# Performance work log

Measured on AMD Instinct MI355X. Metric: run time of the kernel, lower is better.

The kernel has to match this reference:

```python
import jax, jax.numpy as jnp
import numpy as np

IN_FEATURES = 4096
OUT_FEATURES = 4096
GROUP_SIZE = 128
TOKENS = 8192


def setup_inputs() -> dict:
    key = jax.random.key(0)
    k1, k2, k3 = jax.random.split(key, 3)
    x = jax.random.normal(k1, (TOKENS, IN_FEATURES), dtype=jnp.float32)
    weight_packed = jax.random.randint(k2, (OUT_FEATURES, IN_FEATURES // 2), 0, 256, dtype=jnp.int32)
    num_groups = IN_FEATURES // GROUP_SIZE
    weight_scales = jax.random.uniform(k3, (OUT_FEATURES, num_groups), dtype=jnp.float32) * 0.02
    return {"x": x, "weight_packed": weight_packed, "weight_scales": weight_scales, "group_size": GROUP_SIZE}


def _dequantize_int4(packed, scales, group_size):
    # packed: [N, K//2] int (uint8 values); scales: [N, G]
    out_features = packed.shape[0]
    in_features = packed.shape[1] * 2
    low = (packed & 15) - 8   # even columns
    high = ((packed >> 4) & 15) - 8  # odd columns
    # interleave low/high along last axis -> [N, K]
    unpacked = jnp.stack([low, high], axis=-1).reshape(out_features, in_features)
    num_groups = in_features // group_size
    w = unpacked.reshape(out_features, num_groups, group_size).astype(scales.dtype)
    w = w * scales[:, :, None]  # per-group scale
    return w.reshape(out_features, in_features)


def reference(x, weight_packed, weight_scales, group_size):
    W = _dequantize_int4(weight_packed, weight_scales, group_size)  # [N, K]
    # nn.functional.linear: x @ W.T (bias=False)
    return jnp.einsum('tk,nk->tn', x, W)
```

## Files before the change

kernel.cpp:

```cpp
#include <hip/hip_runtime.h>
#include <cstdint>
#include <cstddef>

#define TOKENS 8192
#define IN_F   4096
#define OUT_F  4096

typedef __bf16 bf16;
typedef bf16  bf16x8 __attribute__((ext_vector_type(8)));
typedef float f32x4  __attribute__((ext_vector_type(4)));

__global__ void prep_kernel(const float* __restrict__ xin, bf16* __restrict__ xout,
                            const int* __restrict__ wp, const float* __restrict__ sc,
                            bf16* __restrict__ wout) {
    if (blockIdx.x < 16384) {
        size_t i = ((size_t)blockIdx.x * 256 + threadIdx.x) * 8;
        const float4* p = (const float4*)(xin + i);
        float4 a = p[0], b = p[1];
        bf16x8 r;
        r[0] = (bf16)a.x; r[1] = (bf16)a.y; r[2] = (bf16)a.z; r[3] = (bf16)a.w;
        r[4] = (bf16)b.x; r[5] = (bf16)b.y; r[6] = (bf16)b.z; r[7] = (bf16)b.w;
        *(bf16x8*)(xout + i) = r;
    } else {
        int t  = (blockIdx.x - 16384) * 256 + threadIdx.x;
        int j0 = t << 2;
        int n  = j0 >> 11;
        int g  = (j0 & 2047) >> 6;
        float s = sc[(n << 5) + g];
        int4 p = *(const int4*)(wp + j0);
        bf16x8 r;
        r[0] = (bf16)((float)((p.x & 15) - 8) * s);
        r[1] = (bf16)((float)(((p.x >> 4) & 15) - 8) * s);
        r[2] = (bf16)((float)((p.y & 15) - 8) * s);
        r[3] = (bf16)((float)(((p.y >> 4) & 15) - 8) * s);
        r[4] = (bf16)((float)((p.z & 15) - 8) * s);
        r[5] = (bf16)((float)(((p.z >> 4) & 15) - 8) * s);
        r[6] = (bf16)((float)((p.w & 15) - 8) * s);
        r[7] = (bf16)((float)(((p.w >> 4) & 15) - 8) * s);
        *(bf16x8*)(wout + ((size_t)j0 << 1)) = r;
    }
}


#define GLL(src, dst) __builtin_amdgcn_global_load_lds( \
    (const __attribute__((address_space(1))) void*)(src), \
    (__attribute__((address_space(3))) void*)(dst), 16, 0, 0)
#define BAR() asm volatile("s_barrier" ::: "memory")

__global__ __launch_bounds__(512, 2)
void gemm_kernel(const bf16* __restrict__ A, const bf16* __restrict__ B,
                 float* __restrict__ C) {
    __shared__ char smem[131072] __attribute__((aligned(128)));

    const int tid  = threadIdx.x;
    const int lane = tid & 63;
    const int w    = tid >> 6;
    const int wr   = w >> 2, wc = w & 3;
    const int lrow = lane >> 3;
    const int gsw  = (lane & 7) ^ lrow;

    const int wg = ((blockIdx.x & 7) << 6) | (blockIdx.x >> 3);
    const int mt = wg >> 4;
    const int nt = wg & 15;

    const char* Abase = (const char*)A + (size_t)(mt * 256) * (IN_F * 2);
    const char* Bbase = (const char*)B + (size_t)(nt * 256) * (IN_F * 2);

    const char* gA[4];
#pragma unroll
    for (int t = 0; t < 4; ++t)
        gA[t] = Abase + (size_t)(t * 64 + w * 8 + lrow) * (IN_F * 2) + gsw * 16;
    const int rb = (w >> 2) * 64 + (w & 3) * 8;
    const int brow0 = rb, brow1 = rb + 128, brow2 = rb + 32, brow3 = rb + 160;
    const char* gB[4];
    gB[0] = Bbase + (size_t)(brow0 + lrow) * (IN_F * 2) + gsw * 16;
    gB[1] = Bbase + (size_t)(brow1 + lrow) * (IN_F * 2) + gsw * 16;
    gB[2] = Bbase + (size_t)(brow2 + lrow) * (IN_F * 2) + gsw * 16;
    gB[3] = Bbase + (size_t)(brow3 + lrow) * (IN_F * 2) + gsw * 16;

    char* const sm = smem;
#define ST_A0(b, kt) { GLL(gA[0] + (kt) * 128, sm + (b) * 65536 +     0 + w * 1024); \
                       GLL(gA[2] + (kt) * 128, sm + (b) * 65536 + 16384 + w * 1024); }
#define ST_A1(b, kt) { GLL(gA[1] + (kt) * 128, sm + (b) * 65536 +  8192 + w * 1024); \
                       GLL(gA[3] + (kt) * 128, sm + (b) * 65536 + 24576 + w * 1024); }
#define ST_B0(b, kt) { GLL(gB[0] + (kt) * 128, sm + (b) * 65536 + 32768 + brow0 * 128); \
                       GLL(gB[1] + (kt) * 128, sm + (b) * 65536 + 32768 + brow1 * 128); }
#define ST_B1(b, kt) { GLL(gB[2] + (kt) * 128, sm + (b) * 65536 + 32768 + brow2 * 128); \
                       GLL(gB[3] + (kt) * 128, sm + (b) * 65536 + 32768 + brow3 * 128); }

    const int m_lane = lane & 15, quad = lane >> 4, sw = m_lane & 7;
    const bf16x8* pA0 = (const bf16x8*)sm;
    const bf16x8* pB0 = (const bf16x8*)(sm + 32768);
    const bf16x8* pA1 = (const bf16x8*)(sm + 65536);
    const bf16x8* pB1 = (const bf16x8*)(sm + 98304);

    f32x4 acc[8][4];
#pragma unroll
    for (int i = 0; i < 8; ++i)
#pragma unroll
        for (int j = 0; j < 4; ++j) acc[i][j] = (f32x4)0.0f;

    ST_A0(0, 0); ST_B0(0, 0); ST_B1(0, 0); ST_A1(0, 0);
    ST_A0(1, 1); ST_B0(1, 1); ST_B1(1, 1);
    asm volatile("s_waitcnt vmcnt(6)" ::: "memory");
    BAR();

#define LDA(PA, qr) \
    { _Pragma("unroll") for (int i = 0; i < 4; ++i) { \
        _Pragma("unroll") for (int kh = 0; kh < 2; ++kh) { \
            af[i][kh] = (PA)[(wr * 128 + ((qr) * 4 + i) * 16 + m_lane) * 8 + ((kh * 4 + quad) ^ sw)]; } } }
#define LDB(PB) \
    { _Pragma("unroll") for (int j = 0; j < 4; ++j) { \
        _Pragma("unroll") for (int kh = 0; kh < 2; ++kh) { \
            bfr[j][kh] = (PB)[(wc * 64 + j * 16 + m_lane) * 8 + ((kh * 4 + quad) ^ sw)]; } } }
#define MM(qr, qc) \
    { __builtin_amdgcn_s_setprio(1); \
      _Pragma("unroll") for (int i = 0; i < 4; ++i) { \
        _Pragma("unroll") for (int j = 0; j < 2; ++j) { \
          _Pragma("unroll") for (int kh = 0; kh < 2; ++kh) { \
            acc[(qr) * 4 + i][(qc) * 2 + j] = __builtin_amdgcn_mfma_f32_16x16x32_bf16( \
                af[i][kh], bfr[(qc) * 2 + j][kh], acc[(qr) * 4 + i][(qc) * 2 + j], 0, 0, 0); } } } \
      __builtin_amdgcn_s_setprio(0); }

    for (int it = 0; it < 32; ++it) {
        const int kt0 = 2 * it;
        const int kt1 = kt0 + 1;
        const bool more = (it < 31);
        {
            bf16x8 af[4][2], bfr[4][2];
            LDA(pA0, 0); LDB(pB0);
            ST_A1(1, kt1);
            BAR(); MM(0, 0); BAR();
            if (more) ST_A0(0, kt0 + 2);
            BAR(); MM(0, 1); BAR();
            LDA(pA0, 1);
            if (more) ST_B0(0, kt0 + 2);
            BAR(); MM(1, 0); BAR();
            if (more) ST_B1(0, kt0 + 2);
            if (more) { asm volatile("s_waitcnt vmcnt(6)" ::: "memory"); }
            else      { asm volatile("s_waitcnt vmcnt(0)" ::: "memory"); }
            BAR(); MM(1, 1); BAR();
        }
        {
            bf16x8 af[4][2], bfr[4][2];
            LDA(pA1, 0); LDB(pB1);
            if (more) ST_A1(0, kt1 + 1);
            BAR(); MM(0, 0); BAR();
            if (more) ST_A0(1, kt1 + 2);
            BAR(); MM(0, 1); BAR();
            LDA(pA1, 1);
            if (more) ST_B0(1, kt1 + 2);
            BAR(); MM(1, 0); BAR();
            if (more) ST_B1(1, kt1 + 2);
            if (more) { asm volatile("s_waitcnt vmcnt(6)" ::: "memory"); }
            BAR(); MM(1, 1); BAR();
        }
    }

    const size_t crow0 = (size_t)(mt * 256 + wr * 128 + quad * 4) * OUT_F
                       + (size_t)(nt * 256 + wc * 64 + m_lane);
#pragma unroll
    for (int i = 0; i < 8; ++i)
#pragma unroll
        for (int r = 0; r < 4; ++r) {
            float* cp = C + crow0 + (size_t)(i * 16 + r) * OUT_F;
#pragma unroll
            for (int j = 0; j < 4; ++j) cp[j * 16] = acc[i][j][r];
        }
}

__global__ void naive_kernel(const float* __restrict__ x, const int* __restrict__ wp,
                             const float* __restrict__ sc, float* __restrict__ out) {
    int o = blockIdx.x * 256 + threadIdx.x;
    int t = o >> 12, n = o & 4095;
    const float* xr = x + (size_t)t * IN_F;
    const int*   wr2 = wp + (size_t)n * (IN_F / 2);
    float acc = 0.f;
    for (int g = 0; g < 32; ++g) {
        float s = sc[n * 32 + g];
        float part = 0.f;
        for (int j = 0; j < 64; ++j) {
            int p = wr2[g * 64 + j];
            part += xr[g * 128 + 2 * j]     * (float)((p & 15) - 8);
            part += xr[g * 128 + 2 * j + 1] * (float)(((p >> 4) & 15) - 8);
        }
        acc += part * s;
    }
    out[o] = acc;
}

extern "C" void kernel_launch(void* const* d_in, const int* in_sizes, int n_in,
                              void* d_out, int out_size, void* d_ws, size_t ws_size,
                              hipStream_t stream) {
    const float* x  = (const float*)d_in[0];
    const int*   wp = (const int*)d_in[1];
    const float* sc = (const float*)d_in[2];
    float* out = (float*)d_out;

    const size_t xb_bytes = (size_t)TOKENS * IN_F * 2;
    const size_t wb_bytes = (size_t)OUT_F * IN_F * 2;

    if (ws_size >= xb_bytes + wb_bytes) {
        bf16* xb = (bf16*)d_ws;
        bf16* wb = (bf16*)((char*)d_ws + xb_bytes);
        prep_kernel<<<dim3(16384 + 8192), dim3(256), 0, stream>>>(x, xb, wp, sc, wb);
        gemm_kernel<<<dim3((TOKENS / 256) * (OUT_F / 256)), dim3(512), 0, stream>>>(xb, wb, out);
    } else {
        naive_kernel<<<dim3((TOKENS * OUT_F) / 256), dim3(256), 0, stream>>>(x, wp, sc, out);
    }
}
```

Baseline: 473.9 us.

## Restructure GEMM pipeline with split B-fragment loads and fewer barriers

```diff
diff --git a/kernel.cpp b/kernel.cpp
--- a/kernel.cpp
+++ b/kernel.cpp
@@ -45,7 +45,7 @@
 #define GLL(src, dst) __builtin_amdgcn_global_load_lds( \
     (const __attribute__((address_space(1))) void*)(src), \
     (__attribute__((address_space(3))) void*)(dst), 16, 0, 0)
-#define BAR() asm volatile("s_barrier" ::: "memory")
+#define BARX() { __builtin_amdgcn_s_barrier(); __builtin_amdgcn_sched_barrier(0); }
 
 __global__ __launch_bounds__(512, 2)
 void gemm_kernel(const bf16* __restrict__ A, const bf16* __restrict__ B,
@@ -101,25 +101,25 @@
         for (int j = 0; j < 4; ++j) acc[i][j] = (f32x4)0.0f;
 
     ST_A0(0, 0); ST_B0(0, 0); ST_B1(0, 0); ST_A1(0, 0);
-    ST_A0(1, 1); ST_B0(1, 1); ST_B1(1, 1);
-    asm volatile("s_waitcnt vmcnt(6)" ::: "memory");
-    BAR();
-
-#define LDA(PA, qr) \
+    ST_A0(1, 1); ST_B0(1, 1);
+    asm volatile("s_waitcnt vmcnt(4)" ::: "memory");
+    __builtin_amdgcn_s_barrier();
+
+#define LDA(dst, PA, qr) \
     { _Pragma("unroll") for (int i = 0; i < 4; ++i) { \
         _Pragma("unroll") for (int kh = 0; kh < 2; ++kh) { \
-            af[i][kh] = (PA)[(wr * 128 + ((qr) * 4 + i) * 16 + m_lane) * 8 + ((kh * 4 + quad) ^ sw)]; } } }
-#define LDB(PB) \
-    { _Pragma("unroll") for (int j = 0; j < 4; ++j) { \
+            dst[i][kh] = (PA)[(wr * 128 + ((qr) * 4 + i) * 16 + m_lane) * 8 + ((kh * 4 + quad) ^ sw)]; } } }
+#define LDBq(PB, qc) \
+    { _Pragma("unroll") for (int j = 0; j < 2; ++j) { \
         _Pragma("unroll") for (int kh = 0; kh < 2; ++kh) { \
-            bfr[j][kh] = (PB)[(wc * 64 + j * 16 + m_lane) * 8 + ((kh * 4 + quad) ^ sw)]; } } }
-#define MM(qr, qc) \
+            bfr[(qc) * 2 + j][kh] = (PB)[(wc * 64 + ((qc) * 2 + j) * 16 + m_lane) * 8 + ((kh * 4 + quad) ^ sw)]; } } }
+#define MM(afv, qr, qc) \
     { __builtin_amdgcn_s_setprio(1); \
       _Pragma("unroll") for (int i = 0; i < 4; ++i) { \
         _Pragma("unroll") for (int j = 0; j < 2; ++j) { \
           _Pragma("unroll") for (int kh = 0; kh < 2; ++kh) { \
             acc[(qr) * 4 + i][(qc) * 2 + j] = __builtin_amdgcn_mfma_f32_16x16x32_bf16( \
-                af[i][kh], bfr[(qc) * 2 + j][kh], acc[(qr) * 4 + i][(qc) * 2 + j], 0, 0, 0); } } } \
+                afv[i][kh], bfr[(qc) * 2 + j][kh], acc[(qr) * 4 + i][(qc) * 2 + j], 0, 0, 0); } } } \
       __builtin_amdgcn_s_setprio(0); }
 
     for (int it = 0; it < 32; ++it) {
@@ -127,33 +127,40 @@
         const int kt1 = kt0 + 1;
         const bool more = (it < 31);
         {
-            bf16x8 af[4][2], bfr[4][2];
-            LDA(pA0, 0); LDB(pB0);
+            bf16x8 af0[4][2], af1[4][2], bfr[4][2];
+            LDA(af0, pA0, 0); LDBq(pB0, 0);
+            ST_B1(1, kt1);
+            BARX(); MM(af0, 0, 0);
+            LDBq(pB0, 1);
             ST_A1(1, kt1);
-            BAR(); MM(0, 0); BAR();
+            BARX(); MM(af0, 0, 1);
+            LDA(af1, pA0, 1);
             if (more) ST_A0(0, kt0 + 2);
-            BAR(); MM(0, 1); BAR();
-            LDA(pA0, 1);
-            if (more) ST_B0(0, kt0 + 2);
-            BAR(); MM(1, 0); BAR();
-            if (more) ST_B1(0, kt0 + 2);
-            if (more) { asm volatile("s_waitcnt vmcnt(6)" ::: "memory"); }
-            else      { asm volatile("s_waitcnt vmcnt(0)" ::: "memory"); }
-            BAR(); MM(1, 1); BAR();
+            BARX(); MM(af1, 1, 0);
+            if (more) {
+                ST_B0(0, kt0 + 2);
+                asm volatile("s_waitcnt vmcnt(4)" ::: "memory");
+            } else {
+                asm volatile("s_waitcnt vmcnt(0)" ::: "memory");
+            }
+            BARX(); MM(af1, 1, 1);
         }
         {
-            bf16x8 af[4][2], bfr[4][2];
-            LDA(pA1, 0); LDB(pB1);
+            bf16x8 af0[4][2], af1[4][2], bfr[4][2];
+            LDA(af0, pA1, 0); LDBq(pB1, 0);
+            if (more) ST_B1(0, kt1 + 1);
+            BARX(); MM(af0, 0, 0);
+            LDBq(pB1, 1);
             if (more) ST_A1(0, kt1 + 1);
-            BAR(); MM(0, 0); BAR();
+            BARX(); MM(af0, 0, 1);
+            LDA(af1, pA1, 1);
             if (more) ST_A0(1, kt1 + 2);
-            BAR(); MM(0, 1); BAR();
-            LDA(pA1, 1);
-            if (more) ST_B0(1, kt1 + 2);
-            BAR(); MM(1, 0); BAR();
-            if (more) ST_B1(1, kt1 + 2);
-            if (more) { asm volatile("s_waitcnt vmcnt(6)" ::: "memory"); }
-            BAR(); MM(1, 1); BAR();
+            BARX(); MM(af1, 1, 0);
+            if (more) {
+                ST_B0(1, kt1 + 2);
+                asm volatile("s_waitcnt vmcnt(4)" ::: "memory");
+            }
+            BARX(); MM(af1, 1, 1);
         }
     }
 
```

Measured after the change: 444.3 us. 6.2% less time.
